# Kernel optimization log

Hardware: AMD Instinct MI355X
Metric: run time of the kernel (lower is better)

The kernel has to match this reference:

```python
import jax, jax.numpy as jnp
import numpy as np

C = 512
NUM_GROUPS = 32
EPS = 1e-6


def setup_inputs() -> dict:
    key = jax.random.key(0)
    ks = jax.random.split(key, 10)
    x = jax.random.normal(ks[0], (2, C, 64, 64), dtype=jnp.float32)
    s = 1.0 / np.sqrt(C)
    return {
        "x": x,
        "gn_gamma": jnp.ones((C,), jnp.float32),
        "gn_beta": jnp.zeros((C,), jnp.float32),
        "wq": jax.random.normal(ks[1], (C, C), jnp.float32) * s,
        "bq": jnp.zeros((C,), jnp.float32),
        "wk": jax.random.normal(ks[2], (C, C), jnp.float32) * s,
        "bk": jnp.zeros((C,), jnp.float32),
        "wv": jax.random.normal(ks[3], (C, C), jnp.float32) * s,
        "bv": jnp.zeros((C,), jnp.float32),
        "wo": jax.random.normal(ks[4], (C, C), jnp.float32) * s,
        "bo": jnp.zeros((C,), jnp.float32),
    }


def group_norm(x, gamma, beta):
    b, c, h, w = x.shape
    xg = x.reshape(b, NUM_GROUPS, c // NUM_GROUPS, h, w)
    mean = xg.mean(axis=(2, 3, 4), keepdims=True)
    var = xg.var(axis=(2, 3, 4), keepdims=True)
    xg = (xg - mean) * jax.lax.rsqrt(var + EPS)
    x = xg.reshape(b, c, h, w)
    return x * gamma[None, :, None, None] + beta[None, :, None, None]


def conv1x1(x, w, bias):
    # 1x1 conv == channel matmul: (b,c,h,w),(o,c) -> (b,o,h,w)
    return jnp.einsum('bchw,oc->bohw', x, w) + bias[None, :, None, None]


def reference(x, gn_gamma, gn_beta, wq, bq, wk, bk, wv, bv, wo, bo):
    b, c, h, w = x.shape
    hn = group_norm(x, gn_gamma, gn_beta)
    q = conv1x1(hn, wq, bq).reshape(b, c, h * w)  # (b,c,n)
    k = conv1x1(hn, wk, bk).reshape(b, c, h * w)
    v = conv1x1(hn, wv, bv).reshape(b, c, h * w)
    scale = int(c) ** (-0.5)
    # scores[b,i,j] = sum_c q[b,c,i] k[b,c,j]
    scores = jnp.einsum('bci,bcj->bij', q, k) * scale
    attn = jax.nn.softmax(scores, axis=2)
    out = jnp.einsum('bcj,bij->bci', v, attn).reshape(b, c, h, w)
    out = conv1x1(out, wo, bo)
    return x + out
```

## Files before the change

kernel.cpp:

```cpp
#include <hip/hip_runtime.h>

typedef unsigned short ushort_t;
typedef unsigned char uchar_t;
typedef __bf16 bf16x8 __attribute__((ext_vector_type(8)));
typedef float f32x4 __attribute__((ext_vector_type(4)));

__device__ __forceinline__ ushort_t f2bf(float f) {
  unsigned u = __float_as_uint(f);
  u += 0x7fff + ((u >> 16) & 1);
  return (ushort_t)(u >> 16);
}

__device__ __forceinline__ void gload16(const void* g, void* l) {
  __builtin_amdgcn_global_load_lds(
      (const __attribute__((address_space(1))) unsigned int*)g,
      (__attribute__((address_space(3))) unsigned int*)l, 16, 0, 0);
}

__global__ __launch_bounds__(256) void cvt_weights(
    const float* __restrict__ wq, const float* __restrict__ wk,
    const float* __restrict__ wv, const float* __restrict__ wo,
    const float* __restrict__ bq, const float* __restrict__ bk,
    ushort_t* __restrict__ dst, float* __restrict__ qkbias,
    float* __restrict__ stats2) {
  int b = blockIdx.x, t = threadIdx.x;
  if (b < 1024) {
    int i = b * 256 + t;
    dst[i]          = f2bf(wq[i]);
    dst[262144 + i] = f2bf(wk[i]);
    dst[524288 + i] = f2bf(wv[i]);
    dst[786432 + i] = f2bf(wo[i]);
  } else if (b < 1028) {
    int j = (b - 1024) * 256 + t;
    qkbias[j] = (j < 512) ? bq[j] : bk[j - 512];
  } else {
    if (t < 128) stats2[t] = 0.f;
  }
}

__global__ __launch_bounds__(256) void zero_f32(float* __restrict__ p) {
  p[blockIdx.x * 256 + threadIdx.x] = 0.f;
}

__global__ __launch_bounds__(256) void gn_stats_partial(const float* __restrict__ x,
                                                        float* __restrict__ stats2) {
  int bg = blockIdx.x >> 2, q = blockIdx.x & 3;
  const float4* p = (const float4*)(x + (size_t)bg * 65536 + q * 16384);
  float s = 0.f, ss = 0.f;
  for (int i = threadIdx.x; i < 4096; i += 256) {
    float4 v = p[i];
    s += v.x + v.y + v.z + v.w;
    ss += v.x * v.x + v.y * v.y + v.z * v.z + v.w * v.w;
  }
  for (int off = 32; off; off >>= 1) {
    s += __shfl_xor(s, off, 64);
    ss += __shfl_xor(ss, off, 64);
  }
  __shared__ float sh[8];
  int wave = threadIdx.x >> 6, lane = threadIdx.x & 63;
  if (lane == 0) { sh[wave] = s; sh[4 + wave] = ss; }
  __syncthreads();
  if (threadIdx.x == 0) {
    atomicAdd(&stats2[bg * 2], sh[0] + sh[1] + sh[2] + sh[3]);
    atomicAdd(&stats2[bg * 2 + 1], sh[4] + sh[5] + sh[6] + sh[7]);
  }
}

__global__ __launch_bounds__(64) void gn_finalize(const float* __restrict__ stats2,
                                                  float* __restrict__ stats) {
  int t = threadIdx.x;
  float s = stats2[t * 2], ss = stats2[t * 2 + 1];
  float mean = s * (1.f / 65536.f);
  float var = ss * (1.f / 65536.f) - mean * mean;
  stats[t * 2] = mean;
  stats[t * 2 + 1] = rsqrtf(var + 1e-6f);
}

__global__ __launch_bounds__(256) void gn_apply(
    const float* __restrict__ x, const float* __restrict__ gamma,
    const float* __restrict__ beta, const float* __restrict__ stats,
    ushort_t* __restrict__ hnT) {
  __shared__ float T[32][33];
  int i0 = blockIdx.x * 32, c0 = blockIdx.y * 32, b = blockIdx.z;
  int tx = threadIdx.x, ty = threadIdx.y;
#pragma unroll
  for (int k = 0; k < 4; k++) {
    int cl = ty + k * 8;
    int c = c0 + cl;
    int bg = (b * 32 + (c >> 4)) * 2;
    float mean = stats[bg], rstd = stats[bg + 1];
    float v = x[((size_t)(b * 512 + c)) * 4096 + i0 + tx];
    T[cl][tx] = (v - mean) * rstd * gamma[c] + beta[c];
  }
  __syncthreads();
#pragma unroll
  for (int k = 0; k < 4; k++) {
    int il = ty + k * 8;
    hnT[((size_t)b * 4096 + i0 + il) * 512 + c0 + tx] = f2bf(T[tx][il]);
  }
}

template <int BN, int UNR>
__global__ __launch_bounds__(256) void gemm_abt(
    const ushort_t* __restrict__ A, long long sA, int lda,
    const ushort_t* __restrict__ B, long long sB, int ldb,
    int K, int N, int ldc,
    ushort_t* __restrict__ outB, long long sC,
    const float* __restrict__ bias, int bias_mode, float scale,
    float* __restrict__ outF, const float* __restrict__ resid,
    float* __restrict__ rowsum, const float* __restrict__ colscale,
    int swiz, int omode) {
  constexpr int CPW = (8 + BN / 16) / 4;
  constexpr int SB = (128 + BN) * 32;
  constexpr int STEP = 32 * UNR;
  constexpr int MI = (BN == 128) ? 4 : 2;
  constexpr int NI = 4;
  __shared__ __align__(16) ushort_t Ls[2][UNR * SB];

  int bx = blockIdx.x, by = blockIdx.y, bz = blockIdx.z;
  if (swiz) {
    unsigned nx = gridDim.x, ny = gridDim.y;
    unsigned id = (blockIdx.z * ny + blockIdx.y) * nx + blockIdx.x;
    unsigned pb8 = (nx * ny) >> 3;
    unsigned c = id & 7, j = id >> 3;
    bz = j / pb8;
    unsigned jb = j - bz * pb8;
    unsigned jy = jb / nx;
    by = c * (ny >> 3) + jy;
    bx = jb - jy * nx;
  }

  int m0 = by * 128, n0 = bx * BN;
  int t = threadIdx.x;
  int lane = t & 63;
  int quad = lane >> 4, l16 = lane & 15;
  int wave = t >> 6;
  int wm = (BN == 128) ? (wave >> 1) * 64 : wave * 32;
  int wn = (BN == 128) ? (wave & 1) * 64 : 0;

  f32x4 acc[MI][NI];
#pragma unroll
  for (int i = 0; i < MI; i++)
#pragma unroll
    for (int j = 0; j < NI; j++)
#pragma unroll
      for (int r = 0; r < 4; r++) acc[i][j][r] = 0.f;

  const ushort_t* gp[CPW];
  int lofs[CPW];
  int crow = lane >> 2, skoff = (lane & 3) * 8;
#pragma unroll
  for (int i = 0; i < CPW; i++) {
    int c = wave * CPW + i;
    if (c < 8) {
      gp[i] = A + (size_t)bz * sA + (size_t)(m0 + c * 16 + crow) * lda + skoff;
      lofs[i] = c * 1024 + lane * 16;
    } else {
      int slot = (c - 8) * 16 + crow;
      int arow = (slot & ~63) + ((slot & 15) * 4) + ((slot & 63) >> 4);
      gp[i] = B + (size_t)bz * sB + (size_t)(n0 + arow) * ldb + skoff;
      lofs[i] = 8192 + (c - 8) * 1024 + lane * 16;
    }
  }
  char* lbase = (char*)&Ls[0][0];

#pragma unroll
  for (int s = 0; s < UNR; s++)
#pragma unroll
    for (int i = 0; i < CPW; i++)
      gload16(gp[i] + s * 32, lbase + s * (SB * 2) + lofs[i]);

  for (int k0 = 0; k0 < K; k0 += STEP) {
    int p = (k0 / STEP) & 1;
    __syncthreads();
    if (k0 + STEP < K) {
      int pofs = (p ^ 1) * (UNR * SB * 2);
#pragma unroll
      for (int s = 0; s < UNR; s++)
#pragma unroll
        for (int i = 0; i < CPW; i++)
          gload16(gp[i] + k0 + STEP + s * 32, lbase + pofs + s * (SB * 2) + lofs[i]);
    }
#pragma unroll
    for (int s = 0; s < UNR; s++) {
      bf16x8 af[MI], bfr[NI];
#pragma unroll
      for (int i = 0; i < MI; i++)
        af[i] = *(const bf16x8*)&Ls[p][s * SB + (wm + i * 16 + l16) * 32 + quad * 8];
#pragma unroll
      for (int j = 0; j < NI; j++)
        bfr[j] = *(const bf16x8*)&Ls[p][s * SB + 4096 + (wn + j * 16 + l16) * 32 + quad * 8];
#pragma unroll
      for (int mi = 0; mi < MI; mi++)
#pragma unroll
        for (int ni = 0; ni < NI; ni++)
          acc[mi][ni] = __builtin_amdgcn_mfma_f32_16x16x32_bf16(af[mi], bfr[ni], acc[mi][ni], 0, 0, 0);
    }
  }

  size_t cbase = (size_t)bz * sC;
  int gnb = n0 + wn + l16 * 4;
  float cs4[4] = {1.f, 1.f, 1.f, 1.f};
  if (colscale) {
    float4 c4 = *(const float4*)&colscale[(size_t)bz * N + gnb];
    cs4[0] = 1.f / c4.x; cs4[1] = 1.f / c4.y; cs4[2] = 1.f / c4.z; cs4[3] = 1.f / c4.w;
  }
  float b4[4] = {0.f, 0.f, 0.f, 0.f};
  if (bias_mode == 2) {
    float4 t4 = *(const float4*)&bias[gnb];
    b4[0] = t4.x; b4[1] = t4.y; b4[2] = t4.z; b4[3] = t4.w;
  }
#pragma unroll
  for (int mi = 0; mi < MI; mi++) {
#pragma unroll
    for (int r = 0; r < 4; r++) {
      int m = m0 + wm + mi * 16 + quad * 4 + r;
      float rbias = (bias_mode == 1) ? bias[m] : 0.f;
      float v4[4];
      float rs = 0.f;
#pragma unroll
      for (int ni = 0; ni < NI; ni++) {
        float val = acc[mi][ni][r];
        if (colscale) val *= cs4[ni];
        val += (bias_mode == 2) ? b4[ni] : rbias;
        val *= scale;
        if (rowsum) { val = __expf(val) * 0.0625f; rs += val; }
        v4[ni] = val;
      }
      size_t idx = cbase + (size_t)m * ldc + gnb;
      if (omode == 1) {
        float4 rv = *(const float4*)&resid[idx];
        float4 ov = make_float4(v4[0] + rv.x, v4[1] + rv.y, v4[2] + rv.z, v4[3] + rv.w);
        *(float4*)&outF[idx] = ov;
      } else if (omode == 2) {
        unsigned w = __builtin_amdgcn_cvt_pk_fp8_f32(v4[0], v4[1], 0u, false);
        w = __builtin_amdgcn_cvt_pk_fp8_f32(v4[2], v4[3], w, true);
        *(unsigned*)&((uchar_t*)outB)[idx] = w;
      } else {
        unsigned lo = (unsigned)f2bf(v4[0]) | ((unsigned)f2bf(v4[1]) << 16);
        unsigned hi = (unsigned)f2bf(v4[2]) | ((unsigned)f2bf(v4[3]) << 16);
        *(uint2*)&outB[idx] = make_uint2(lo, hi);
      }
      if (rowsum) {
        rs += __shfl_xor(rs, 1, 64);
        rs += __shfl_xor(rs, 2, 64);
        rs += __shfl_xor(rs, 4, 64);
        rs += __shfl_xor(rs, 8, 64);
        if (l16 == 0) atomicAdd(&rowsum[(size_t)bz * 4096 + m], rs);
      }
    }
  }
}

__global__ __launch_bounds__(256) void gemm_qk(
    const uchar_t* __restrict__ A, long long sA, int lda,
    const uchar_t* __restrict__ B, long long sB, int ldb,
    int K, int ldc, uchar_t* __restrict__ outp, long long sC,
    float scale, float* __restrict__ rowsum) {
  constexpr int ABY = 16384;
  constexpr int SBB = ABY + 8192;
  constexpr int CPW = 6;
  __shared__ __align__(16) uchar_t Ls[2][SBB];

  unsigned nx = gridDim.x, ny = gridDim.y;
  unsigned id = (blockIdx.z * ny + blockIdx.y) * nx + blockIdx.x;
  unsigned pb8 = (nx * ny) >> 3;
  unsigned cc = id & 7, j = id >> 3;
  int bz = j / pb8;
  unsigned jb = j - bz * pb8;
  unsigned jy = jb / nx;
  int by = cc * (ny >> 3) + jy;
  int bx = jb - jy * nx;

  int m0 = by * 256, n0 = bx * 128;
  int t = threadIdx.x;
  int lane = t & 63;
  int quad = lane >> 4, l16 = lane & 15;
  int wave = t >> 6;
  int wm = (wave >> 1) * 64, wn = (wave & 1) * 64;

  f32x4 acc[2][4][4];
#pragma unroll
  for (int h = 0; h < 2; h++)
#pragma unroll
    for (int i = 0; i < 4; i++)
#pragma unroll
      for (int j4 = 0; j4 < 4; j4++)
#pragma unroll
        for (int r = 0; r < 4; r++) acc[h][i][j4][r] = 0.f;

  const uchar_t* gp[CPW];
  int lofs[CPW];
  int r16 = lane & 15, sseg = quad * 16;
#pragma unroll
  for (int i = 0; i < CPW; i++) {
    int c = wave * CPW + i;
    if (c < 16) {
      gp[i] = A + (size_t)bz * sA + (size_t)(m0 + c * 16 + r16) * lda + sseg;
      lofs[i] = c * 1024 + lane * 16;
    } else {
      int cb = c - 16;
      int slot = cb * 16 + r16;
      int arow = (slot & ~63) + ((slot & 15) * 4) + ((slot & 63) >> 4);
      gp[i] = B + (size_t)bz * sB + (size_t)(n0 + arow) * ldb + sseg;
      lofs[i] = ABY + cb * 1024 + lane * 16;
    }
  }
  char* lbase = (char*)&Ls[0][0];

#pragma unroll
  for (int i = 0; i < CPW; i++) gload16(gp[i], lbase + lofs[i]);

  int vbase = l16 * 16 + (quad >> 1) * 256 + (quad & 1) * 8;
  for (int k0 = 0; k0 < K; k0 += 64) {
    int p = (k0 >> 6) & 1;
    __syncthreads();
    if (k0 + 64 < K) {
      int pofs = (p ^ 1) * SBB;
#pragma unroll
      for (int i = 0; i < CPW; i++)
        gload16(gp[i] + k0 + 64, lbase + pofs + lofs[i]);
    }
    const uchar_t* Lp = &Ls[p][0];
#pragma unroll
    for (int s = 0; s < 2; s++) {
      long long af[2][4], bfv[4];
#pragma unroll
      for (int h = 0; h < 2; h++)
#pragma unroll
        for (int i = 0; i < 4; i++)
          af[h][i] = *(const long long*)&Lp[h * 8192 + wm * 64 + i * 1024 + s * 512 + vbase];
#pragma unroll
      for (int j4 = 0; j4 < 4; j4++)
        bfv[j4] = *(const long long*)&Lp[ABY + wn * 64 + j4 * 1024 + s * 512 + vbase];
#pragma unroll
      for (int h = 0; h < 2; h++)
#pragma unroll
        for (int mi = 0; mi < 4; mi++)
#pragma unroll
          for (int ni = 0; ni < 4; ni++)
            acc[h][mi][ni] = __builtin_amdgcn_mfma_f32_16x16x32_fp8_fp8(af[h][mi], bfv[ni], acc[h][mi][ni], 0, 0, 0);
    }
  }

  size_t cbase = (size_t)bz * sC;
  int gnb = n0 + wn + l16 * 4;
#pragma unroll
  for (int h = 0; h < 2; h++) {
#pragma unroll
    for (int mi = 0; mi < 4; mi++) {
#pragma unroll
      for (int r = 0; r < 4; r++) {
        int m = m0 + h * 128 + wm + mi * 16 + quad * 4 + r;
        float v4[4];
        float rs = 0.f;
#pragma unroll
        for (int ni = 0; ni < 4; ni++) {
          v4[ni] = __expf(acc[h][mi][ni][r] * scale) * 0.0625f;
          rs += v4[ni];
        }
        unsigned w = __builtin_amdgcn_cvt_pk_fp8_f32(v4[0], v4[1], 0u, false);
        w = __builtin_amdgcn_cvt_pk_fp8_f32(v4[2], v4[3], w, true);
        *(unsigned*)&outp[cbase + (size_t)m * ldc + gnb] = w;
        rs += __shfl_xor(rs, 1, 64);
        rs += __shfl_xor(rs, 2, 64);
        rs += __shfl_xor(rs, 4, 64);
        rs += __shfl_xor(rs, 8, 64);
        if (l16 == 0) atomicAdd(&rowsum[(size_t)bz * 4096 + m], rs);
      }
    }
  }
}

__global__ __launch_bounds__(256) void gemm_pv(
    const uchar_t* __restrict__ A, long long sA, int lda,
    const uchar_t* __restrict__ B, long long sB, int ldb,
    int K, int ldc, ushort_t* __restrict__ outp, long long sC) {
  constexpr int BASEB = 32768;
  constexpr int SBB = BASEB + 8192;
  constexpr int NL = SBB / 4096;
  __shared__ __align__(16) uchar_t Ls[2][SBB];

  unsigned nx = gridDim.x, ny = gridDim.y;
  unsigned id = (blockIdx.z * ny + blockIdx.y) * nx + blockIdx.x;
  unsigned pb8 = (nx * ny) >> 3;
  unsigned cc = id & 7, j = id >> 3;
  int bz = j / pb8;
  unsigned jb = j - bz * pb8;
  unsigned jy = jb / nx;
  int by = cc * (ny >> 3) + jy;
  int bx = jb - jy * nx;

  int m0 = by * 256, n0 = bx * 64;
  int t = threadIdx.x;
  int lane = t & 63;
  int quad = lane >> 4, l16 = lane & 15;
  int wave = t >> 6;
  int wm = wave * 32;

  f32x4 acc[2][2][4];
#pragma unroll
  for (int h = 0; h < 2; h++)
#pragma unroll
    for (int i = 0; i < 2; i++)
#pragma unroll
      for (int j4 = 0; j4 < 4; j4++)
#pragma unroll
        for (int r = 0; r < 4; r++) acc[h][i][j4][r] = 0.f;

  const uchar_t* gp[NL];
  int lofs[NL];
#pragma unroll
  for (int i = 0; i < NL; i++) {
    int o = i * 4096 + t * 16;
    int row = o >> 7;
    int kb = (o & 127) ^ ((row & 7) << 4);
    if (row < 256) {
      gp[i] = A + (size_t)bz * sA + (size_t)(m0 + row) * lda + kb;
    } else {
      int br = row - 256;
      int ar = (br & 15) * 4 + (br >> 4);
      gp[i] = B + (size_t)bz * sB + (size_t)(n0 + ar) * ldb + kb;
    }
    lofs[i] = o;
  }
  char* lbase = (char*)&Ls[0][0];

  const int NT = K >> 7;
#pragma unroll
  for (int i = 0; i < NL; i++) gload16(gp[i], lbase + lofs[i]);
#pragma unroll
  for (int i = 0; i < NL; i++) gload16(gp[i] + 128, lbase + SBB + lofs[i]);

  int swz = (l16 & 7) << 4;
  for (int kt = 0; kt < NT; ++kt) {
    if (kt < NT - 1)
      asm volatile("s_waitcnt vmcnt(10)" ::: "memory");
    else
      asm volatile("s_waitcnt vmcnt(0)" ::: "memory");
    __builtin_amdgcn_s_barrier();
    const uchar_t* Lp = &Ls[kt & 1][0];
    __builtin_amdgcn_s_setprio(1);
#pragma unroll
    for (int ks = 0; ks < 4; ks++) {
      int kx = (ks * 32 + quad * 8) ^ swz;
      long long af[2][2], bfv[4];
#pragma unroll
      for (int h = 0; h < 2; h++)
#pragma unroll
        for (int i = 0; i < 2; i++)
          af[h][i] = *(const long long*)&Lp[(h * 128 + wm + i * 16 + l16) * 128 + kx];
#pragma unroll
      for (int j4 = 0; j4 < 4; j4++)
        bfv[j4] = *(const long long*)&Lp[BASEB + (j4 * 16 + l16) * 128 + kx];
#pragma unroll
      for (int h = 0; h < 2; h++)
#pragma unroll
        for (int mi = 0; mi < 2; mi++)
#pragma unroll
          for (int ni = 0; ni < 4; ni++)
            acc[h][mi][ni] = __builtin_amdgcn_mfma_f32_16x16x32_fp8_fp8(af[h][mi], bfv[ni], acc[h][mi][ni], 0, 0, 0);
    }
    __builtin_amdgcn_s_setprio(0);
    if (kt + 2 < NT) {
      asm volatile("s_waitcnt lgkmcnt(0)" ::: "memory");
      __builtin_amdgcn_sched_barrier(0);
      __builtin_amdgcn_s_barrier();
      int pofs = (kt & 1) * SBB;
      int ko = (kt + 2) * 128;
#pragma unroll
      for (int i = 0; i < NL; i++)
        gload16(gp[i] + ko, lbase + pofs + lofs[i]);
    }
  }

  size_t cbase = (size_t)bz * sC;
  int gnb = n0 + l16 * 4;
#pragma unroll
  for (int h = 0; h < 2; h++) {
#pragma unroll
    for (int mi = 0; mi < 2; mi++) {
#pragma unroll
      for (int r = 0; r < 4; r++) {
        int m = m0 + h * 128 + wm + mi * 16 + quad * 4 + r;
        unsigned lo = (unsigned)f2bf(acc[h][mi][0][r]) | ((unsigned)f2bf(acc[h][mi][1][r]) << 16);
        unsigned hi = (unsigned)f2bf(acc[h][mi][2][r]) | ((unsigned)f2bf(acc[h][mi][3][r]) << 16);
        *(uint2*)&outp[cbase + (size_t)m * ldc + gnb] = make_uint2(lo, hi);
      }
    }
  }
}

extern "C" void kernel_launch(void* const* d_in, const int* in_sizes, int n_in,
                              void* d_out, int out_size, void* d_ws, size_t ws_size,
                              hipStream_t stream) {
  const float* x     = (const float*)d_in[0];
  const float* gamma = (const float*)d_in[1];
  const float* beta  = (const float*)d_in[2];
  const float* wq    = (const float*)d_in[3];
  const float* bq    = (const float*)d_in[4];
  const float* wk    = (const float*)d_in[5];
  const float* bk    = (const float*)d_in[6];
  const float* wv    = (const float*)d_in[7];
  const float* bv    = (const float*)d_in[8];
  const float* wo    = (const float*)d_in[9];
  const float* bo    = (const float*)d_in[10];
  float* out = (float*)d_out;

  ushort_t* wb  = (ushort_t*)d_ws;
  ushort_t* wvb = wb + 524288;
  ushort_t* wob = wb + 786432;
  ushort_t* hnT = wb + 1048576;
  uchar_t*  qk8 = (uchar_t*)(hnT + 4194304);
  uchar_t*  vC8 = qk8 + 8388608;
  ushort_t* OT  = (ushort_t*)(vC8 + 4194304);
  uchar_t*  S8  = (uchar_t*)(OT + 4194304);
  float* fbuf   = (float*)(S8 + 33554432);
  float* stats  = fbuf;
  float* stats2 = fbuf + 128;
  float* qkbias = fbuf + 256;
  float* l      = (float*)hnT;

  const long long HS = 2097152;
  const long long QS = 4194304;
  const long long SS = 16777216;
  const float scale = 0.044194173824159216f;

  cvt_weights<<<dim3(1029), dim3(256), 0, stream>>>(wq, wk, wv, wo, bq, bk, wb, qkbias, stats2);
  gn_stats_partial<<<dim3(256), dim3(256), 0, stream>>>(x, stats2);
  gn_finalize<<<dim3(1), dim3(64), 0, stream>>>(stats2, stats);
  gn_apply<<<dim3(128, 16, 2), dim3(32, 8), 0, stream>>>(x, gamma, beta, stats, hnT);
  gemm_abt<128, 2><<<dim3(8, 32, 2), dim3(256), 0, stream>>>(
      hnT, HS, 512, wb, 0, 512, 512, 1024, 1024, (ushort_t*)qk8, QS, qkbias, 2, 1.f,
      nullptr, nullptr, nullptr, nullptr, 1, 2);
  gemm_abt<64, 2><<<dim3(64, 4, 2), dim3(256), 0, stream>>>(
      wvb, 0, 512, hnT, HS, 512, 512, 4096, 4096, (ushort_t*)vC8, HS, bv, 1, 1.f,
      nullptr, nullptr, nullptr, nullptr, 0, 2);
  zero_f32<<<dim3(32), dim3(256), 0, stream>>>(l);
  gemm_qk<<<dim3(32, 16, 2), dim3(256), 0, stream>>>(
      qk8, QS, 1024, qk8 + 512, QS, 1024, 512, 4096, S8, SS, scale, l);
  gemm_pv<<<dim3(8, 16, 2), dim3(256), 0, stream>>>(
      S8, SS, 4096, vC8, HS, 4096, 4096, 512, OT, HS);
  gemm_abt<64, 2><<<dim3(64, 4, 2), dim3(256), 0, stream>>>(
      wob, 0, 512, OT, HS, 512, 512, 4096, 4096, nullptr, HS, bo, 1, 1.f,
      out, x, nullptr, l, 0, 1);
}
```

Before: 259.0 us.

## Shrink QK tile to 128x128 and prefetch two stages with explicit waitcnt

The QK^T GEMM tile is halved from 256x128 to 128x128, which doubles the grid and cuts accumulator registers to raise occupancy. The k-loop is reworked to issue loads two tiles ahead into the double buffer, gating each tile with s_waitcnt vmcnt rather than a plain syncthreads. It also raises wave priority around the MFMA block. The trade-off is more blocks re-reading the same B tiles, plus an extra barrier per iteration to protect buffer reuse.

```diff
diff --git a/kernel.cpp b/kernel.cpp
--- a/kernel.cpp
+++ b/kernel.cpp
@@ -257,9 +257,9 @@
     const uchar_t* __restrict__ B, long long sB, int ldb,
     int K, int ldc, uchar_t* __restrict__ outp, long long sC,
     float scale, float* __restrict__ rowsum) {
-  constexpr int ABY = 16384;
-  constexpr int SBB = ABY + 8192;
-  constexpr int CPW = 6;
+  constexpr int SBB = 16384;
+  constexpr int BASEB = 8192;
+  constexpr int NL = 4;
   __shared__ __align__(16) uchar_t Ls[2][SBB];
 
   unsigned nx = gridDim.x, ny = gridDim.y;
@@ -272,102 +272,104 @@
   int by = cc * (ny >> 3) + jy;
   int bx = jb - jy * nx;
 
-  int m0 = by * 256, n0 = bx * 128;
+  int m0 = by * 128, n0 = bx * 128;
   int t = threadIdx.x;
   int lane = t & 63;
   int quad = lane >> 4, l16 = lane & 15;
   int wave = t >> 6;
   int wm = (wave >> 1) * 64, wn = (wave & 1) * 64;
 
-  f32x4 acc[2][4][4];
-#pragma unroll
-  for (int h = 0; h < 2; h++)
-#pragma unroll
-    for (int i = 0; i < 4; i++)
-#pragma unroll
-      for (int j4 = 0; j4 < 4; j4++)
-#pragma unroll
-        for (int r = 0; r < 4; r++) acc[h][i][j4][r] = 0.f;
-
-  const uchar_t* gp[CPW];
-  int lofs[CPW];
+  f32x4 acc[4][4];
+#pragma unroll
+  for (int i = 0; i < 4; i++)
+#pragma unroll
+    for (int j4 = 0; j4 < 4; j4++)
+#pragma unroll
+      for (int r = 0; r < 4; r++) acc[i][j4][r] = 0.f;
+
+  const uchar_t* gp[NL];
+  int lofs[NL];
   int r16 = lane & 15, sseg = quad * 16;
 #pragma unroll
-  for (int i = 0; i < CPW; i++) {
-    int c = wave * CPW + i;
-    if (c < 16) {
+  for (int i = 0; i < NL; i++) {
+    int c = wave * NL + i;
+    if (c < 8) {
       gp[i] = A + (size_t)bz * sA + (size_t)(m0 + c * 16 + r16) * lda + sseg;
       lofs[i] = c * 1024 + lane * 16;
     } else {
-      int cb = c - 16;
-      int slot = cb * 16 + r16;
+      int slot = (c - 8) * 16 + r16;
       int arow = (slot & ~63) + ((slot & 15) * 4) + ((slot & 63) >> 4);
       gp[i] = B + (size_t)bz * sB + (size_t)(n0 + arow) * ldb + sseg;
-      lofs[i] = ABY + cb * 1024 + lane * 16;
+      lofs[i] = BASEB + (c - 8) * 1024 + lane * 16;
     }
   }
   char* lbase = (char*)&Ls[0][0];
 
-#pragma unroll
-  for (int i = 0; i < CPW; i++) gload16(gp[i], lbase + lofs[i]);
+  const int NT = K >> 6;
+#pragma unroll
+  for (int i = 0; i < NL; i++) gload16(gp[i], lbase + lofs[i]);
+#pragma unroll
+  for (int i = 0; i < NL; i++) gload16(gp[i] + 64, lbase + SBB + lofs[i]);
 
   int vbase = l16 * 16 + (quad >> 1) * 256 + (quad & 1) * 8;
-  for (int k0 = 0; k0 < K; k0 += 64) {
-    int p = (k0 >> 6) & 1;
-    __syncthreads();
-    if (k0 + 64 < K) {
-      int pofs = (p ^ 1) * SBB;
-#pragma unroll
-      for (int i = 0; i < CPW; i++)
-        gload16(gp[i] + k0 + 64, lbase + pofs + lofs[i]);
-    }
-    const uchar_t* Lp = &Ls[p][0];
+  for (int kt = 0; kt < NT; ++kt) {
+    if (kt < NT - 1)
+      asm volatile("s_waitcnt vmcnt(4)" ::: "memory");
+    else
+      asm volatile("s_waitcnt vmcnt(0)" ::: "memory");
+    __builtin_amdgcn_s_barrier();
+    const uchar_t* Lp = &Ls[kt & 1][0];
+    __builtin_amdgcn_s_setprio(1);
 #pragma unroll
     for (int s = 0; s < 2; s++) {
-      long long af[2][4], bfv[4];
-#pragma unroll
-      for (int h = 0; h < 2; h++)
-#pragma unroll
-        for (int i = 0; i < 4; i++)
-          af[h][i] = *(const long long*)&Lp[h * 8192 + wm * 64 + i * 1024 + s * 512 + vbase];
+      long long af[4], bfv[4];
+#pragma unroll
+      for (int i = 0; i < 4; i++)
+        af[i] = *(const long long*)&Lp[wm * 64 + i * 1024 + s * 512 + vbase];
 #pragma unroll
       for (int j4 = 0; j4 < 4; j4++)
-        bfv[j4] = *(const long long*)&Lp[ABY + wn * 64 + j4 * 1024 + s * 512 + vbase];
-#pragma unroll
-      for (int h = 0; h < 2; h++)
-#pragma unroll
-        for (int mi = 0; mi < 4; mi++)
-#pragma unroll
-          for (int ni = 0; ni < 4; ni++)
-            acc[h][mi][ni] = __builtin_amdgcn_mfma_f32_16x16x32_fp8_fp8(af[h][mi], bfv[ni], acc[h][mi][ni], 0, 0, 0);
+        bfv[j4] = *(const long long*)&Lp[BASEB + wn * 64 + j4 * 1024 + s * 512 + vbase];
+#pragma unroll
+      for (int mi = 0; mi < 4; mi++)
+#pragma unroll
+        for (int ni = 0; ni < 4; ni++)
+          acc[mi][ni] = __builtin_amdgcn_mfma_f32_16x16x32_fp8_fp8(af[mi], bfv[ni], acc[mi][ni], 0, 0, 0);
+    }
+    __builtin_amdgcn_s_setprio(0);
+    if (kt + 2 < NT) {
+      asm volatile("s_waitcnt lgkmcnt(0)" ::: "memory");
+      __builtin_amdgcn_sched_barrier(0);
+      __builtin_amdgcn_s_barrier();
+      int pofs = (kt & 1) * SBB;
+      int ko = (kt + 2) * 64;
+#pragma unroll
+      for (int i = 0; i < NL; i++)
+        gload16(gp[i] + ko, lbase + pofs + lofs[i]);
     }
   }
 
   size_t cbase = (size_t)bz * sC;
   int gnb = n0 + wn + l16 * 4;
 #pragma unroll
-  for (int h = 0; h < 2; h++) {
-#pragma unroll
-    for (int mi = 0; mi < 4; mi++) {
-#pragma unroll
-      for (int r = 0; r < 4; r++) {
-        int m = m0 + h * 128 + wm + mi * 16 + quad * 4 + r;
-        float v4[4];
-        float rs = 0.f;
-#pragma unroll
-        for (int ni = 0; ni < 4; ni++) {
-          v4[ni] = __expf(acc[h][mi][ni][r] * scale) * 0.0625f;
-          rs += v4[ni];
-        }
-        unsigned w = __builtin_amdgcn_cvt_pk_fp8_f32(v4[0], v4[1], 0u, false);
-        w = __builtin_amdgcn_cvt_pk_fp8_f32(v4[2], v4[3], w, true);
-        *(unsigned*)&outp[cbase + (size_t)m * ldc + gnb] = w;
-        rs += __shfl_xor(rs, 1, 64);
-        rs += __shfl_xor(rs, 2, 64);
-        rs += __shfl_xor(rs, 4, 64);
-        rs += __shfl_xor(rs, 8, 64);
-        if (l16 == 0) atomicAdd(&rowsum[(size_t)bz * 4096 + m], rs);
+  for (int mi = 0; mi < 4; mi++) {
+#pragma unroll
+    for (int r = 0; r < 4; r++) {
+      int m = m0 + wm + mi * 16 + quad * 4 + r;
+      float v4[4];
+      float rs = 0.f;
+#pragma unroll
+      for (int ni = 0; ni < 4; ni++) {
+        v4[ni] = __expf(acc[mi][ni][r] * scale) * 0.0625f;
+        rs += v4[ni];
       }
+      unsigned w = __builtin_amdgcn_cvt_pk_fp8_f32(v4[0], v4[1], 0u, false);
+      w = __builtin_amdgcn_cvt_pk_fp8_f32(v4[2], v4[3], w, true);
+      *(unsigned*)&outp[cbase + (size_t)m * ldc + gnb] = w;
+      rs += __shfl_xor(rs, 1, 64);
+      rs += __shfl_xor(rs, 2, 64);
+      rs += __shfl_xor(rs, 4, 64);
+      rs += __shfl_xor(rs, 8, 64);
+      if (l16 == 0) atomicAdd(&rowsum[(size_t)bz * 4096 + m], rs);
     }
   }
 }
@@ -537,7 +539,7 @@
       wvb, 0, 512, hnT, HS, 512, 512, 4096, 4096, (ushort_t*)vC8, HS, bv, 1, 1.f,
       nullptr, nullptr, nullptr, nullptr, 0, 2);
   zero_f32<<<dim3(32), dim3(256), 0, stream>>>(l);
-  gemm_qk<<<dim3(32, 16, 2), dim3(256), 0, stream>>>(
+  gemm_qk<<<dim3(32, 32, 2), dim3(256), 0, stream>>>(
       qk8, QS, 1024, qk8 + 512, QS, 1024, 512, 4096, S8, SS, scale, l);
   gemm_pv<<<dim3(8, 16, 2), dim3(256), 0, stream>>>(
       S8, SS, 4096, vC8, HS, 4096, 4096, 512, OT, HS);
```

New measurement: 236.0 us. 1.1x faster.
